# Optimization experiments

Hardware: AMD Instinct MI355X
Metric: run time of the kernel (lower is better)

The kernel has to match this reference:

```python
import jax, jax.numpy as jnp
import numpy as np

B=64; HW=14; E=2048; L=30; V=10000; EMB=512; AML=768; ADL=500
D=512+ADL   # decoder_dim + article_downlen = 1012
A=512+ADL   # attention_dim + article_downlen = 1012

def setup_inputs() -> dict:
    key = jax.random.key(0)
    ks = jax.random.split(key, 20)
    s = 0.02
    lin = lambda k, i, o: (jax.random.normal(k, (i, o), jnp.float32) * s)
    inp = {}
    inp['encoder_out'] = jax.random.normal(ks[0], (B, HW, HW, E), jnp.float32)
    inp['encoded_captions'] = jax.random.randint(ks[1], (B, L), 0, V)
    cl = jax.random.randint(ks[2], (B, 1), 2, L + 1)
    inp['caption_lengths'] = cl.at[0, 0].set(L)  # ensure max decode length == L-1
    inp['encoded_articles'] = jax.random.normal(ks[3], (B, 1, AML), jnp.float32)
    inp['article_lengths'] = jax.random.randint(ks[4], (B, 1), 1, AML)
    inp['blank_context'] = 0
    inp['E_emb'] = jax.random.uniform(ks[5], (V, EMB), jnp.float32, -0.1, 0.1)
    inp['W_par'] = lin(ks[6], AML, ADL); inp['b_par'] = jnp.zeros(ADL, jnp.float32)
    inp['W_enc'] = lin(ks[7], E, A);     inp['b_enc'] = jnp.zeros(A, jnp.float32)
    inp['W_dec'] = lin(ks[8], D, A);     inp['b_dec'] = jnp.zeros(A, jnp.float32)
    inp['W_full'] = lin(ks[9], A, 1);    inp['b_full'] = jnp.zeros(1, jnp.float32)
    inp['W_h'] = lin(ks[10], E + ADL, D); inp['b_h'] = jnp.zeros(D, jnp.float32)
    inp['W_c'] = lin(ks[11], E + ADL, D); inp['b_c'] = jnp.zeros(D, jnp.float32)
    inp['W_fb'] = lin(ks[12], D, E);      inp['b_fb'] = jnp.zeros(E, jnp.float32)
    inp['W_ih'] = lin(ks[13], EMB + E, 4 * D); inp['b_ih'] = jnp.zeros(4 * D, jnp.float32)
    inp['W_hh'] = lin(ks[14], D, 4 * D);       inp['b_hh'] = jnp.zeros(4 * D, jnp.float32)
    inp['W_fc'] = jax.random.uniform(ks[15], (D, V), jnp.float32, -0.1, 0.1)
    inp['b_fc'] = jnp.zeros(V, jnp.float32)
    return inp

def reference(encoder_out, encoded_captions, caption_lengths, encoded_articles,
              article_lengths, blank_context, E_emb, W_par, b_par, W_enc, b_enc,
              W_dec, b_dec, W_full, b_full, W_h, b_h, W_c, b_c, W_fb, b_fb,
              W_ih, b_ih, W_hh, b_hh, W_fc, b_fc):
    Bv = encoder_out.shape[0]
    enc = encoder_out.reshape(Bv, -1, encoder_out.shape[-1])  # (B, P, E)
    lens = caption_lengths[:, 0]
    sort_ind = jnp.argsort(-lens)
    lens = lens[sort_ind]
    enc = enc[sort_ind]
    caps = encoded_captions[sort_ind]
    arts = encoded_articles[sort_ind]
    emb = E_emb[caps]                                   # (B, L, EMB)
    context = (arts @ W_par + b_par)[:, 0, :]           # ParagraphEncoder -> (B, ADL)
    dec_in = jnp.concatenate([enc.mean(axis=1), context], axis=1)
    h0 = dec_in @ W_h + b_h
    c0 = dec_in @ W_c + b_c
    dlens = lens - 1
    att1 = enc @ W_enc + b_enc                          # loop-invariant, (B, P, A)
    T = emb.shape[1] - 1

    def step(carry, t):
        h, c = carry
        active = (dlens > t)[:, None]                   # prefix mask (sorted desc)
        att2 = h @ W_dec + b_dec
        scores = (jax.nn.relu(att1 + att2[:, None, :]) @ W_full)[..., 0] + b_full[0]
        alpha = jax.nn.softmax(scores, axis=1)          # (B, P)
        awe = jnp.einsum('bp,bpe->be', alpha, enc)
        awe = jax.nn.sigmoid(h @ W_fb + b_fb) * awe     # gated attention encoding
        x = jnp.concatenate([emb[:, t, :], awe], axis=1)
        gates = x @ W_ih + b_ih + h @ W_hh + b_hh       # torch LSTMCell, gate order i,f,g,o
        i, f, g, o = jnp.split(gates, 4, axis=1)
        c_new = jax.nn.sigmoid(f) * c + jax.nn.sigmoid(i) * jnp.tanh(g)
        h_new = jax.nn.sigmoid(o) * jnp.tanh(c_new)
        preds = jnp.where(active, h_new @ W_fc + b_fc, 0.0)
        alpha_m = jnp.where(active, alpha, 0.0)
        h = jnp.where(active, h_new, h)
        c = jnp.where(active, c_new, c)
        return (h, c), (preds, alpha_m)

    _, (preds, alphas) = jax.lax.scan(step, (h0, c0), jnp.arange(T))
    predictions = jnp.transpose(preds, (1, 0, 2))       # (B, T, V)
    alphas = jnp.transpose(alphas, (1, 0, 2))           # (B, T, P)
    return (predictions, caps, dlens, alphas, sort_ind)
```

## Files before the change

### kernel.cpp

```cpp
#include <hip/hip_runtime.h>
#include <math.h>

#define B_   64
#define P_   196
#define E_   2048
#define L_   30
#define T_   29
#define V_   10000
#define EMB_ 512
#define AML_ 768
#define ADL_ 500
#define D_   1012
#define A_   1012
#define G4_  4048
#define XK_  2560

typedef unsigned short u16;
typedef __attribute__((ext_vector_type(8))) short bf16x8;
typedef __attribute__((ext_vector_type(4))) float f32x4;

__device__ __forceinline__ float sigf(float x) { return 1.f / (1.f + __expf(-x)); }
__device__ __forceinline__ float tanhf_fast(float x) { return 1.f - 2.f / (__expf(2.f * x) + 1.f); }
__device__ __forceinline__ u16 f2bf(float f) {
    unsigned u = __float_as_uint(f);
    return (u16)((u + 0x7FFFu + ((u >> 16) & 1u)) >> 16);
}
__device__ __forceinline__ float bf2f(u16 v) { return __uint_as_float(((unsigned)v) << 16); }

__global__ void k_setup(const int* __restrict__ clen, const int* __restrict__ caps,
                        float* __restrict__ out_caps, float* __restrict__ out_dlens,
                        float* __restrict__ out_sind,
                        int* __restrict__ sort_ind, int* __restrict__ dlens_i,
                        int* __restrict__ nact, int* __restrict__ caps_s)
{
    __shared__ int lens[B_];
    int t = threadIdx.x;
    if (t < B_) lens[t] = clen[t];
    __syncthreads();
    if (t < B_) {
        int my = lens[t];
        int rank = 0;
        for (int j = 0; j < B_; ++j) {
            int lj = lens[j];
            if (lj > my || (lj == my && j < t)) rank++;
        }
        sort_ind[rank] = t;
    }
    __syncthreads();
    if (t < B_) {
        int orig = sort_ind[t];
        int dl = lens[orig] - 1;
        dlens_i[t] = dl;
        out_dlens[t] = (float)dl;
        out_sind[t] = (float)orig;
        for (int j = 0; j < L_; ++j) {
            int cv = caps[orig * L_ + j];
            caps_s[t * L_ + j] = cv;
            out_caps[t * L_ + j] = (float)cv;
        }
    }
    __syncthreads();
    if (t < T_) {
        int cnt = 0;
        for (int j = 0; j < B_; ++j) cnt += (dlens_i[j] > t) ? 1 : 0;
        nact[t] = cnt;
    }
}

__global__ void k_zero(float4* __restrict__ p, long n4)
{
    long i = (long)blockIdx.x * 256 + threadIdx.x;
    if (i < n4) p[i] = make_float4(0.f, 0.f, 0.f, 0.f);
}

__global__ void k_cvt_enc(const float* __restrict__ enc, const int* __restrict__ sort_ind,
                          u16* __restrict__ A_bf)
{
    int row = blockIdx.y;
    int b = row / 196, p = row - b * 196;
    int e4 = (blockIdx.x * 256 + threadIdx.x) * 4;
    const float* src = enc + ((long)sort_ind[b] * 196 + p) * E_ + e4;
    float4 v = *(const float4*)src;
    unsigned lo = (unsigned)f2bf(v.x) | ((unsigned)f2bf(v.y) << 16);
    unsigned hi = (unsigned)f2bf(v.z) | ((unsigned)f2bf(v.w) << 16);
    uint2 pk; pk.x = lo; pk.y = hi;
    *(uint2*)(A_bf + (long)row * E_ + e4) = pk;
}

__global__ void k_transpose(const float* __restrict__ src, u16* __restrict__ dst,
                            int K, int N, int Kp, int Np)
{
    __shared__ float tile[32][33];
    int n0 = blockIdx.x * 32, k0 = blockIdx.y * 32;
    int tx = threadIdx.x, ty = threadIdx.y;
    for (int r = ty; r < 32; r += 8) {
        int k = k0 + r, n = n0 + tx;
        tile[r][tx] = (k < K && n < N) ? src[(long)k * N + n] : 0.f;
    }
    __syncthreads();
    for (int r = ty; r < 32; r += 8) {
        int n = n0 + r, k = k0 + tx;
        if (n < Np && k < Kp) dst[(long)n * Kp + k] = f2bf(tile[tx][r]);
    }
}

__global__ void k_encmean(const float* __restrict__ enc, const int* __restrict__ sort_ind,
                          u16* __restrict__ dec_in)
{
    int b = blockIdx.y;
    int e = blockIdx.x * 256 + threadIdx.x;
    int orig = sort_ind[b];
    const float* src = enc + (long)orig * P_ * E_ + e;
    float s = 0.f;
    for (int p = 0; p < P_; ++p) s += src[(long)p * E_];
    dec_in[(long)b * XK_ + e] = f2bf(s * (1.f / 196.f));
}

__global__ void k_ctx(const float* __restrict__ arts, const float* __restrict__ W_par,
                      const float* __restrict__ b_par, const int* __restrict__ sort_ind,
                      u16* __restrict__ dec_in)
{
    int b = blockIdx.y;
    int k = blockIdx.x * 256 + threadIdx.x;
    if (k >= 512) return;
    float s = 0.f;
    if (k < ADL_) {
        int orig = sort_ind[b];
        const float* ar = arts + (long)orig * AML_;
        s = b_par[k];
        for (int m = 0; m < AML_; ++m) s = fmaf(ar[m], W_par[m * ADL_ + k], s);
    }
    dec_in[(long)b * XK_ + E_ + k] = f2bf(s);
}

__global__ void k_emb_all(const float* __restrict__ E_emb, const int* __restrict__ caps_s,
                          u16* __restrict__ emb_all)
{
    int t = blockIdx.x;
    int b = blockIdx.y;
    int tok = caps_s[b * L_ + t];
    for (int k = threadIdx.x; k < EMB_; k += 256)
        emb_all[((long)t * B_ + b) * EMB_ + k] = f2bf(E_emb[(long)tok * EMB_ + k]);
}

__global__ void __launch_bounds__(256) k_att1_mfma(
    const u16* __restrict__ A, const u16* __restrict__ W,
    const float* __restrict__ bias, u16* __restrict__ Yb)
{
    int w = threadIdx.x >> 6, lane = threadIdx.x & 63;
    int lr = lane & 15, lk = (lane >> 4) * 8;
    int n0 = blockIdx.x * 256 + w * 64;
    int r0 = blockIdx.y * 64;
    f32x4 acc[4][4];
#pragma unroll
    for (int i = 0; i < 4; ++i)
#pragma unroll
        for (int j = 0; j < 4; ++j) acc[i][j] = (f32x4){0.f, 0.f, 0.f, 0.f};
    const u16* ap = A + (long)(r0 + lr) * E_ + lk;
    const u16* wp = W + (long)(n0 + lr) * E_ + lk;
    for (int k = 0; k < E_; k += 32) {
        bf16x8 af[4], bf[4];
#pragma unroll
        for (int mt = 0; mt < 4; ++mt) af[mt] = *(const bf16x8*)(ap + (long)mt * 16 * E_ + k);
#pragma unroll
        for (int nt = 0; nt < 4; ++nt) bf[nt] = *(const bf16x8*)(wp + (long)nt * 16 * E_ + k);
#pragma unroll
        for (int mt = 0; mt < 4; ++mt)
#pragma unroll
            for (int nt = 0; nt < 4; ++nt)
                acc[mt][nt] = __builtin_amdgcn_mfma_f32_16x16x32_bf16(af[mt], bf[nt], acc[mt][nt], 0, 0, 0);
    }
#pragma unroll
    for (int mt = 0; mt < 4; ++mt) {
#pragma unroll
        for (int nt = 0; nt < 4; ++nt) {
            int n = n0 + nt * 16 + lr;
            float bv = (n < A_) ? bias[n] : 0.f;
#pragma unroll
            for (int j = 0; j < 4; ++j) {
                int row = r0 + mt * 16 + (lane >> 4) * 4 + j;
                u16 outv = (n < A_) ? f2bf(acc[mt][nt][j] + bv) : (u16)0;
                Yb[(long)row * 1024 + n] = outv;
            }
        }
    }
}

template <int ACT, int OUT, int PADZ>
__global__ void __launch_bounds__(256) k_skinny(
    const u16* __restrict__ A1, const u16* __restrict__ W1, int K1,
    const float* __restrict__ bias1, void* __restrict__ Yv,
    long ldY, long offY, int Nmax,
    const int* __restrict__ nact, int t)
{
    int Bact = (t >= 0) ? nact[t] : B_;
    if (Bact <= 0) return;
    int mmax = (Bact + 15) >> 4;
    int w = threadIdx.x >> 6, lane = threadIdx.x & 63;
    int lr = lane & 15, lk = (lane >> 4) * 8;
    int n0 = blockIdx.x * 64 + w * 16;
    f32x4 acc[4];
#pragma unroll
    for (int m = 0; m < 4; ++m) acc[m] = (f32x4){0.f, 0.f, 0.f, 0.f};

    int n = n0 + lr;
    int nc = n < Nmax ? n : Nmax - 1;
    const u16* a1p = A1 + (long)lr * K1 + lk;
    const u16* w1p = W1 + (long)nc * K1 + lk;
    for (int k = 0; k < K1; k += 32) {
        bf16x8 bw = *(const bf16x8*)(w1p + k);
#pragma unroll
        for (int m = 0; m < 4; ++m)
            if (m < mmax) {
                bf16x8 aw = *(const bf16x8*)(a1p + (long)m * 16 * K1 + k);
                acc[m] = __builtin_amdgcn_mfma_f32_16x16x32_bf16(aw, bw, acc[m], 0, 0, 0);
            }
    }
    float bv = (n < Nmax) ? bias1[n] : 0.f;
#pragma unroll
    for (int m = 0; m < 4; ++m) {
        if (m < mmax) {
#pragma unroll
            for (int j = 0; j < 4; ++j) {
                int b = m * 16 + (lane >> 4) * 4 + j;
                if (b < Bact) {
                    float v = acc[m][j] + bv;
                    if (ACT == 1) v = sigf(v);
                    if (n < Nmax) {
                        if (OUT == 1) ((u16*)Yv)[(long)b * ldY + offY + n] = f2bf(v);
                        else          ((float*)Yv)[(long)b * ldY + offY + n] = v;
                    } else if (PADZ) {
                        if (OUT == 1) ((u16*)Yv)[(long)b * ldY + offY + n] = 0;
                        else          ((float*)Yv)[(long)b * ldY + offY + n] = 0.f;
                    }
                }
            }
        }
    }
}

__global__ void __launch_bounds__(256) k_att2fb(
    const u16* __restrict__ h_bf, const u16* __restrict__ WT_dec,
    const u16* __restrict__ WT_fb, const float* __restrict__ b_dec,
    const float* __restrict__ b_fb, float* __restrict__ att2p,
    float* __restrict__ fbp, const int* __restrict__ nact, int t)
{
    int Bact = nact[t];
    if (Bact <= 0) return;
    int mmax = (Bact + 15) >> 4;
    int kh = blockIdx.x >= 48;
    int nb = blockIdx.x - (kh ? 48 : 0);
    int isfb = nb >= 16;
    const u16* W = isfb ? WT_fb : WT_dec;
    const float* bias = isfb ? b_fb : b_dec;
    int Nmax = isfb ? E_ : A_;
    int nb2 = isfb ? nb - 16 : nb;
    long ldY = isfb ? (long)E_ : 1024L;
    float* Y = (isfb ? fbp : att2p) + (long)kh * B_ * ldY;

    int w = threadIdx.x >> 6, lane = threadIdx.x & 63;
    int lr = lane & 15, lk = (lane >> 4) * 8;
    int n = nb2 * 64 + w * 16 + lr;
    int nc = n < Nmax ? n : Nmax - 1;
    int k0 = kh * 512;
    f32x4 acc[4];
#pragma unroll
    for (int m = 0; m < 4; ++m) acc[m] = (f32x4){0.f, 0.f, 0.f, 0.f};
    const u16* ap = h_bf + (long)lr * 1024 + k0 + lk;
    const u16* wp = W + (long)nc * 1024 + k0 + lk;
    for (int k = 0; k < 512; k += 32) {
        bf16x8 bw = *(const bf16x8*)(wp + k);
#pragma unroll
        for (int m = 0; m < 4; ++m)
            if (m < mmax) {
                bf16x8 aw = *(const bf16x8*)(ap + (long)m * 16 * 1024 + k);
                acc[m] = __builtin_amdgcn_mfma_f32_16x16x32_bf16(aw, bw, acc[m], 0, 0, 0);
            }
    }
    if (n >= Nmax) return;
    float bv = (kh == 0) ? bias[n] : 0.f;
#pragma unroll
    for (int m = 0; m < 4; ++m) {
        if (m < mmax) {
#pragma unroll
            for (int j = 0; j < 4; ++j) {
                int b = m * 16 + (lane >> 4) * 4 + j;
                if (b < Bact) Y[(long)b * ldY + n] = acc[m][j] + bv;
            }
        }
    }
}

__global__ void k_scores(const u16* __restrict__ att1, const float* __restrict__ att2p,
                         const float* __restrict__ W_full, const float* __restrict__ b_full,
                         float* __restrict__ scores, const int* __restrict__ nact, int t)
{
    int b = blockIdx.y;
    if (b >= nact[t]) return;
    int wv = threadIdx.x >> 6;
    int lane = threadIdx.x & 63;
    int p = blockIdx.x * 4 + wv;
    const u16* a1 = att1 + ((long)b * P_ + p) * 1024;
    const float* a20 = att2p + (long)b * 1024;
    const float* a21 = att2p + (long)B_ * 1024 + (long)b * 1024;
    float acc = 0.f;
    for (int j2 = lane; j2 < 506; j2 += 64) {
        unsigned pk = *(const unsigned*)(a1 + 2 * j2);
        float2 p0 = *(const float2*)(a20 + 2 * j2);
        float2 p1 = *(const float2*)(a21 + 2 * j2);
        float2 wv2 = *(const float2*)(W_full + 2 * j2);
        float v0 = bf2f((u16)(pk & 0xFFFF)) + p0.x + p1.x;
        float v1 = bf2f((u16)(pk >> 16)) + p0.y + p1.y;
        v0 = v0 > 0.f ? v0 : 0.f;
        v1 = v1 > 0.f ? v1 : 0.f;
        acc = fmaf(v0, wv2.x, acc);
        acc = fmaf(v1, wv2.y, acc);
    }
    for (int m = 32; m >= 1; m >>= 1) acc += __shfl_xor(acc, m);
    if (lane == 0) scores[b * P_ + p] = acc + b_full[0];
}

__global__ void __launch_bounds__(256) k_awe_x(
    const u16* __restrict__ A_bf, const float* __restrict__ scores,
    const float* __restrict__ fbp, u16* __restrict__ awe_buf,
    float* __restrict__ alphas_out, const int* __restrict__ nact, int t)
{
    int b = blockIdx.y;
    if (b >= nact[t]) return;
    int tid = threadIdx.x;
    int w = tid >> 6, lane = tid & 63;
    __shared__ float al[P_];
    __shared__ float red[4];
    float v = (tid < P_) ? scores[b * P_ + tid] : -1e30f;
    float m = v;
    for (int s = 32; s >= 1; s >>= 1) m = fmaxf(m, __shfl_xor(m, s));
    if (lane == 0) red[w] = m;
    __syncthreads();
    m = fmaxf(fmaxf(red[0], red[1]), fmaxf(red[2], red[3]));
    float e = (tid < P_) ? __expf(v - m) : 0.f;
    float s_ = e;
    for (int s = 32; s >= 1; s >>= 1) s_ += __shfl_xor(s_, s);
    __syncthreads();
    if (lane == 0) red[w] = s_;
    __syncthreads();
    s_ = red[0] + red[1] + red[2] + red[3];
    if (tid < P_) al[tid] = e / s_;
    __syncthreads();

    if (blockIdx.x < 8) {
        int e0 = blockIdx.x * 256 + tid;
        const u16* src = A_bf + (long)b * P_ * E_ + e0;
        float s0 = 0.f, s1 = 0.f, s2 = 0.f, s3 = 0.f;
        for (int p = 0; p < P_; p += 4) {
            s0 = fmaf(al[p],     bf2f(src[(long)p * E_]), s0);
            s1 = fmaf(al[p + 1], bf2f(src[(long)(p + 1) * E_]), s1);
            s2 = fmaf(al[p + 2], bf2f(src[(long)(p + 2) * E_]), s2);
            s3 = fmaf(al[p + 3], bf2f(src[(long)(p + 3) * E_]), s3);
        }
        float g = sigf(fbp[(long)b * E_ + e0] + fbp[(long)(B_ + b) * E_ + e0]);
        awe_buf[(long)b * E_ + e0] = f2bf((s0 + s1 + s2 + s3) * g);
    } else {
        if (tid < P_) alphas_out[((long)b * T_ + t) * P_ + tid] = al[tid];
    }
}

__global__ void __launch_bounds__(256) k_gates(
    const u16* __restrict__ emb_t, const u16* __restrict__ awe,
    const u16* __restrict__ h_old, const u16* __restrict__ WT_ih,
    const u16* __restrict__ WT_hh, float* __restrict__ gpart,
    const int* __restrict__ nact, int t)
{
    int Bact = nact[t];
    if (Bact <= 0) return;
    int mmax = (Bact + 15) >> 4;
    int q = threadIdx.x >> 6;
    int lane = threadIdx.x & 63;
    int lr = lane & 15, lk = (lane >> 4) * 8;
    int kh = blockIdx.y;
    int n = blockIdx.x * 16 + lr;
    int nc = n < D_ ? n : D_ - 1;
    f32x4 acc[4];
#pragma unroll
    for (int m = 0; m < 4; ++m) acc[m] = (f32x4){0.f, 0.f, 0.f, 0.f};
    const u16* wih = WT_ih + ((long)q * D_ + nc) * XK_;
    const u16* whh = WT_hh + ((long)q * D_ + nc) * 1024;

    if (kh == 0) {
        const u16* ap = emb_t + (long)lr * EMB_ + lk;
        for (int k = 0; k < EMB_; k += 32) {
            bf16x8 bw = *(const bf16x8*)(wih + k);
#pragma unroll
            for (int m = 0; m < 4; ++m)
                if (m < mmax) {
                    bf16x8 aw = *(const bf16x8*)(ap + (long)m * 16 * EMB_ + k);
                    acc[m] = __builtin_amdgcn_mfma_f32_16x16x32_bf16(aw, bw, acc[m], 0, 0, 0);
                }
        }
        const u16* ap2 = awe + (long)lr * E_ + lk;
        const u16* w2 = wih + EMB_;
        for (int k = 0; k < 1280; k += 32) {
            bf16x8 bw = *(const bf16x8*)(w2 + k);
#pragma unroll
            for (int m = 0; m < 4; ++m)
                if (m < mmax) {
                    bf16x8 aw = *(const bf16x8*)(ap2 + (long)m * 16 * E_ + k);
                    acc[m] = __builtin_amdgcn_mfma_f32_16x16x32_bf16(aw, bw, acc[m], 0, 0, 0);
                }
        }
    } else {
        const u16* ap2 = awe + (long)lr * E_ + 1280 + lk;
        const u16* w2 = wih + 1792;
        for (int k = 0; k < 768; k += 32) {
            bf16x8 bw = *(const bf16x8*)(w2 + k);
#pragma unroll
            for (int m = 0; m < 4; ++m)
                if (m < mmax) {
                    bf16x8 aw = *(const bf16x8*)(ap2 + (long)m * 16 * E_ + k);
                    acc[m] = __builtin_amdgcn_mfma_f32_16x16x32_bf16(aw, bw, acc[m], 0, 0, 0);
                }
        }
        const u16* ap3 = h_old + (long)lr * 1024 + lk;
        for (int k = 0; k < 1024; k += 32) {
            bf16x8 bw = *(const bf16x8*)(whh + k);
#pragma unroll
            for (int m = 0; m < 4; ++m)
                if (m < mmax) {
                    bf16x8 aw = *(const bf16x8*)(ap3 + (long)m * 16 * 1024 + k);
                    acc[m] = __builtin_amdgcn_mfma_f32_16x16x32_bf16(aw, bw, acc[m], 0, 0, 0);
                }
        }
    }
#pragma unroll
    for (int m = 0; m < 4; ++m) {
        if (m < mmax) {
#pragma unroll
            for (int j = 0; j < 4; ++j) {
                int bb = m * 16 + (lane >> 4) * 4 + j;
                if (bb < Bact)
                    gpart[((long)kh * B_ + bb) * 4096 + q * 1024 + n] = acc[m][j];
            }
        }
    }
}

__global__ void k_lstm_red(const float* __restrict__ gpart, const float* __restrict__ b_ih,
                           const float* __restrict__ b_hh, float* __restrict__ cbuf,
                           u16* __restrict__ h_new, const int* __restrict__ nact, int t)
{
    int b = blockIdx.y;
    if (b >= nact[t]) return;
    int n = blockIdx.x * 256 + threadIdx.x;
    if (n >= D_) return;
    const float* g0 = gpart + (long)b * 4096;
    const float* g1 = gpart + (long)(B_ + b) * 4096;
    float gi = g0[n]        + g1[n]        + b_ih[n]          + b_hh[n];
    float gf = g0[1024 + n] + g1[1024 + n] + b_ih[D_ + n]     + b_hh[D_ + n];
    float gg = g0[2048 + n] + g1[2048 + n] + b_ih[2 * D_ + n] + b_hh[2 * D_ + n];
    float go = g0[3072 + n] + g1[3072 + n] + b_ih[3 * D_ + n] + b_hh[3 * D_ + n];
    float c = cbuf[(long)b * 1024 + n];
    float cn = sigf(gf) * c + sigf(gi) * tanhf_fast(gg);
    float hn = sigf(go) * tanhf_fast(cn);
    cbuf[(long)b * 1024 + n] = cn;
    h_new[(long)b * 1024 + n] = f2bf(hn);
}

__global__ void __launch_bounds__(256) k_fc_all(
    const u16* __restrict__ h_all, const u16* __restrict__ W,
    const float* __restrict__ bias, float* __restrict__ out_preds,
    const int* __restrict__ nact)
{
    int tslot = blockIdx.y;
    int Bact = nact[tslot];
    if (Bact <= 0) return;
    int mmax = (Bact + 15) >> 4;
    int w = threadIdx.x >> 6, lane = threadIdx.x & 63;
    int lr = lane & 15, lk = (lane >> 4) * 8;
    int n0 = blockIdx.x * 256 + w * 64;
    f32x4 acc[4][4];
#pragma unroll
    for (int i = 0; i < 4; ++i)
#pragma unroll
        for (int j = 0; j < 4; ++j) acc[i][j] = (f32x4){0.f, 0.f, 0.f, 0.f};
    const u16* ap = h_all + ((long)(tslot + 1) * B_ + lr) * 1024 + lk;
    int ncl[4];
#pragma unroll
    for (int nt = 0; nt < 4; ++nt) {
        int n = n0 + nt * 16 + lr;
        ncl[nt] = n < V_ ? n : V_ - 1;
    }
    for (int k = 0; k < 1024; k += 32) {
        bf16x8 af[4], bf[4];
#pragma unroll
        for (int mt = 0; mt < 4; ++mt)
            if (mt < mmax) af[mt] = *(const bf16x8*)(ap + (long)mt * 16 * 1024 + k);
#pragma unroll
        for (int nt = 0; nt < 4; ++nt) bf[nt] = *(const bf16x8*)(W + (long)ncl[nt] * 1024 + lk + k);
#pragma unroll
        for (int mt = 0; mt < 4; ++mt)
            if (mt < mmax)
#pragma unroll
                for (int nt = 0; nt < 4; ++nt)
                    acc[mt][nt] = __builtin_amdgcn_mfma_f32_16x16x32_bf16(af[mt], bf[nt], acc[mt][nt], 0, 0, 0);
    }
#pragma unroll
    for (int nt = 0; nt < 4; ++nt) {
        int n = n0 + nt * 16 + lr;
        if (n >= V_) continue;
        float bv = bias[n];
#pragma unroll
        for (int mt = 0; mt < 4; ++mt) {
            if (mt < mmax) {
#pragma unroll
                for (int j = 0; j < 4; ++j) {
                    int b = mt * 16 + (lane >> 4) * 4 + j;
                    if (b < Bact)
                        out_preds[(long)b * T_ * V_ + (long)tslot * V_ + n] = acc[mt][nt][j] + bv;
                }
            }
        }
    }
}

extern "C" void kernel_launch(void* const* d_in, const int* in_sizes, int n_in,
                              void* d_out, int out_size, void* d_ws, size_t ws_size,
                              hipStream_t stream)
{
    const float* enc    = (const float*)d_in[0];
    const int*   caps   = (const int*)d_in[1];
    const int*   clen   = (const int*)d_in[2];
    const float* arts   = (const float*)d_in[3];
    const float* E_emb  = (const float*)d_in[6];
    const float* W_par  = (const float*)d_in[7];
    const float* b_par  = (const float*)d_in[8];
    const float* W_enc  = (const float*)d_in[9];
    const float* b_enc  = (const float*)d_in[10];
    const float* W_dec  = (const float*)d_in[11];
    const float* b_dec  = (const float*)d_in[12];
    const float* W_full = (const float*)d_in[13];
    const float* b_full = (const float*)d_in[14];
    const float* W_h    = (const float*)d_in[15];
    const float* b_h    = (const float*)d_in[16];
    const float* W_c    = (const float*)d_in[17];
    const float* b_c    = (const float*)d_in[18];
    const float* W_fb   = (const float*)d_in[19];
    const float* b_fb   = (const float*)d_in[20];
    const float* W_ih   = (const float*)d_in[21];
    const float* b_ih   = (const float*)d_in[22];
    const float* W_hh   = (const float*)d_in[23];
    const float* b_hh   = (const float*)d_in[24];
    const float* W_fc   = (const float*)d_in[25];
    const float* b_fc   = (const float*)d_in[26];

    float* out = (float*)d_out;
    float* out_preds  = out;
    float* out_caps   = out + (long)B_ * T_ * V_;
    float* out_dlens  = out_caps + B_ * L_;
    float* out_alphas = out_dlens + B_;
    float* out_sind   = out_alphas + (long)B_ * T_ * P_;

    float* ws = (float*)d_ws;
    long o = 0;
    auto alloc = [&](long n) { long r = o; o += (n + 63) & ~63L; return r; };
    long o_ints   = alloc(2176);
    long o_decin  = alloc((long)B_ * XK_ / 2);
    long o_hall   = alloc((long)(T_ + 1) * B_ * 1024 / 2);
    long o_emball = alloc((long)T_ * B_ * EMB_ / 2);
    long o_awe    = alloc((long)B_ * E_ / 2);
    long o_c      = alloc((long)B_ * 1024);
    long o_att2p  = alloc((long)2 * B_ * 1024);
    long o_fbp    = alloc((long)2 * B_ * E_);
    long o_gpart  = alloc((long)2 * B_ * 4096);
    long o_scores = alloc((long)B_ * P_);
    long o_Abf    = alloc((long)12544 * E_ / 2);
    long o_att1   = alloc((long)12544 * 1024 / 2);
    long o_wtenc  = alloc((long)1024 * 2048 / 2);
    long o_wtdec  = alloc((long)1024 * 1024 / 2);
    long o_wtfb   = alloc((long)2048 * 1024 / 2);
    long o_wtih   = alloc((long)4096 * 2560 / 2);
    long o_wthh   = alloc((long)4096 * 1024 / 2);
    long o_wtfc   = alloc((long)10048 * 1024 / 2);

    int* sort_ind = (int*)(ws + o_ints);
    int* dlens_i  = sort_ind + 64;
    int* nact     = dlens_i + 64;
    int* caps_s   = nact + 32;
    u16*   dec_in  = (u16*)(ws + o_decin);
    u16*   h_all   = (u16*)(ws + o_hall);
    u16*   emb_all = (u16*)(ws + o_emball);
    u16*   awe_buf = (u16*)(ws + o_awe);
    float* cbuf   = ws + o_c;
    float* att2p  = ws + o_att2p;
    float* fbp    = ws + o_fbp;
    float* gpart  = ws + o_gpart;
    float* scores = ws + o_scores;
    u16*   A_bf   = (u16*)(ws + o_Abf);
    u16*   att1   = (u16*)(ws + o_att1);
    u16*   WT_enc = (u16*)(ws + o_wtenc);
    u16*   WT_dec = (u16*)(ws + o_wtdec);
    u16*   WT_fb  = (u16*)(ws + o_wtfb);
    u16*   WT_ih  = (u16*)(ws + o_wtih);
    u16*   WT_hh  = (u16*)(ws + o_wthh);
    u16*   WT_fc  = (u16*)(ws + o_wtfc);
    u16*   WT_h   = att1;
    u16*   WT_c   = att1 + (long)1024 * XK_;

    long n4 = ((long)B_ * T_ * V_ + B_ * L_ + B_ + (long)B_ * T_ * P_ + B_) / 4;
    k_zero<<<dim3((unsigned)((n4 + 255) / 256)), 256, 0, stream>>>((float4*)d_out, n4);
    k_setup<<<1, 64, 0, stream>>>(clen, caps, out_caps, out_dlens, out_sind,
                                  sort_ind, dlens_i, nact, caps_s);

    k_encmean<<<dim3(8, 64), 256, 0, stream>>>(enc, sort_ind, dec_in);
    k_ctx<<<dim3(2, 64), 256, 0, stream>>>(arts, W_par, b_par, sort_ind, dec_in);
    k_emb_all<<<dim3(T_, 64), 256, 0, stream>>>(E_emb, caps_s, emb_all);

    dim3 tb(32, 8);
    k_transpose<<<dim3(1024/32, 2560/32), tb, 0, stream>>>(W_h, WT_h, 2548, 1012, 2560, 1024);
    k_transpose<<<dim3(1024/32, 2560/32), tb, 0, stream>>>(W_c, WT_c, 2548, 1012, 2560, 1024);
    k_skinny<0,1,1><<<dim3(16), 256, 0, stream>>>(dec_in, WT_h, XK_, b_h, h_all, 1024L, 0L, D_,
                                                  nact, -1);
    k_skinny<0,0,1><<<dim3(16), 256, 0, stream>>>(dec_in, WT_c, XK_, b_c, cbuf, 1024L, 0L, D_,
                                                  nact, -1);

    k_transpose<<<dim3(1024/32, 2048/32), tb, 0, stream>>>(W_enc, WT_enc, 2048, 1012, 2048, 1024);
    k_transpose<<<dim3(1024/32, 1024/32), tb, 0, stream>>>(W_dec, WT_dec, 1012, 1012, 1024, 1024);
    k_transpose<<<dim3(2048/32, 1024/32), tb, 0, stream>>>(W_fb, WT_fb, 1012, 2048, 1024, 2048);
    k_transpose<<<dim3(4096/32, 2560/32), tb, 0, stream>>>(W_ih, WT_ih, 2560, 4048, 2560, 4096);
    k_transpose<<<dim3(4096/32, 1024/32), tb, 0, stream>>>(W_hh, WT_hh, 1012, 4048, 1024, 4096);
    k_transpose<<<dim3(10048/32, 1024/32), tb, 0, stream>>>(W_fc, WT_fc, 1012, 10000, 1024, 10048);

    k_cvt_enc<<<dim3(2, 12544), 256, 0, stream>>>(enc, sort_ind, A_bf);
    k_att1_mfma<<<dim3(4, 196), 256, 0, stream>>>(A_bf, WT_enc, b_enc, att1);

    for (int t = 0; t < T_; ++t) {
        const u16* h_old = h_all + (long)t * B_ * 1024;
        u16* h_new = h_all + (long)(t + 1) * B_ * 1024;
        const u16* emb_t = emb_all + (long)t * B_ * EMB_;
        k_att2fb<<<dim3(96), 256, 0, stream>>>(h_old, WT_dec, WT_fb, b_dec, b_fb,
                                               att2p, fbp, nact, t);
        k_scores<<<dim3(49, 64), 256, 0, stream>>>(att1, att2p, W_full, b_full, scores, nact, t);
        k_awe_x<<<dim3(9, 64), 256, 0, stream>>>(A_bf, scores, fbp, awe_buf,
                                                 out_alphas, nact, t);
        k_gates<<<dim3(64, 2), 256, 0, stream>>>(emb_t, awe_buf, h_old, WT_ih, WT_hh,
                                                 gpart, nact, t);
        k_lstm_red<<<dim3(4, 64), 256, 0, stream>>>(gpart, b_ih, b_hh, cbuf, h_new, nact, t);
    }
    k_fc_all<<<dim3(40, T_), 256, 0, stream>>>(h_all, WT_fc, b_fc, out_preds, nact);
}
```

Measured before the change: 3.111 ms.

## Precompute embedding gate contributions for all steps; stage att1 A tiles in LDS

The embedding part of the LSTM input projection (emb @ W_ih[:512]) does not depend on the recurrence, so it is now computed for all timesteps in one batched MFMA kernel before the loop. The per-step gate kernel only handles the attention-weighted encoding and hidden-state terms, with its K split rebalanced between the two block halves, and the LSTM reduction adds the precomputed term. The att1 GEMM now double-buffers A tiles through shared memory so the four waves share them instead of each loading them from global memory. The cost is an extra T*B*4096 float workspace and extra synchronisation in the att1 loop.

Result: faster. 2.847 ms (-8.5%).

```diff
diff --git a/kernel.cpp b/kernel.cpp
--- a/kernel.cpp
+++ b/kernel.cpp
@@ -147,28 +147,42 @@
     const u16* __restrict__ A, const u16* __restrict__ W,
     const float* __restrict__ bias, u16* __restrict__ Yb)
 {
+    __shared__ u16 As[2][64][40];
     int w = threadIdx.x >> 6, lane = threadIdx.x & 63;
     int lr = lane & 15, lk = (lane >> 4) * 8;
     int n0 = blockIdx.x * 256 + w * 64;
     int r0 = blockIdx.y * 64;
+    int arow = threadIdx.x >> 2;
+    int akseg = (threadIdx.x & 3) * 8;
+    const u16* ag = A + (long)(r0 + arow) * E_ + akseg;
+
     f32x4 acc[4][4];
 #pragma unroll
     for (int i = 0; i < 4; ++i)
 #pragma unroll
         for (int j = 0; j < 4; ++j) acc[i][j] = (f32x4){0.f, 0.f, 0.f, 0.f};
-    const u16* ap = A + (long)(r0 + lr) * E_ + lk;
     const u16* wp = W + (long)(n0 + lr) * E_ + lk;
+
+    *(uint2*)&As[0][arow][akseg] = *(const uint2*)(ag);
+    __syncthreads();
+
     for (int k = 0; k < E_; k += 32) {
-        bf16x8 af[4], bf[4];
-#pragma unroll
-        for (int mt = 0; mt < 4; ++mt) af[mt] = *(const bf16x8*)(ap + (long)mt * 16 * E_ + k);
+        int buf = (k >> 5) & 1;
+        bool more = (k + 32) < E_;
+        uint2 pre;
+        if (more) pre = *(const uint2*)(ag + k + 32);
+        bf16x8 bf[4], af[4];
 #pragma unroll
         for (int nt = 0; nt < 4; ++nt) bf[nt] = *(const bf16x8*)(wp + (long)nt * 16 * E_ + k);
+#pragma unroll
+        for (int mt = 0; mt < 4; ++mt) af[mt] = *(const bf16x8*)&As[buf][mt * 16 + lr][lk];
 #pragma unroll
         for (int mt = 0; mt < 4; ++mt)
 #pragma unroll
             for (int nt = 0; nt < 4; ++nt)
                 acc[mt][nt] = __builtin_amdgcn_mfma_f32_16x16x32_bf16(af[mt], bf[nt], acc[mt][nt], 0, 0, 0);
+        if (more) *(uint2*)&As[buf ^ 1][arow][akseg] = pre;
+        __syncthreads();
     }
 #pragma unroll
     for (int mt = 0; mt < 4; ++mt) {
@@ -234,6 +248,53 @@
                         else          ((float*)Yv)[(long)b * ldY + offY + n] = 0.f;
                     }
                 }
+            }
+        }
+    }
+}
+
+__global__ void __launch_bounds__(256) k_gemb(
+    const u16* __restrict__ emb_all, const u16* __restrict__ WT_ih,
+    float* __restrict__ gemb_all)
+{
+    int t = blockIdx.y;
+    int w = threadIdx.x >> 6, lane = threadIdx.x & 63;
+    int lr = lane & 15, lk = (lane >> 4) * 8;
+    int n0 = blockIdx.x * 256 + w * 64;
+    f32x4 acc[4][4];
+#pragma unroll
+    for (int i = 0; i < 4; ++i)
+#pragma unroll
+        for (int j = 0; j < 4; ++j) acc[i][j] = (f32x4){0.f, 0.f, 0.f, 0.f};
+    const u16* ap = emb_all + ((long)t * B_ + lr) * EMB_ + lk;
+    long wrow[4];
+#pragma unroll
+    for (int nt = 0; nt < 4; ++nt) {
+        int j = n0 + nt * 16 + lr;
+        int q = j >> 10, d = j & 1023;
+        wrow[nt] = (long)q * D_ + (d < D_ ? d : D_ - 1);
+    }
+    for (int k = 0; k < EMB_; k += 32) {
+        bf16x8 af[4], bf[4];
+#pragma unroll
+        for (int mt = 0; mt < 4; ++mt) af[mt] = *(const bf16x8*)(ap + (long)mt * 16 * EMB_ + k);
+#pragma unroll
+        for (int nt = 0; nt < 4; ++nt) bf[nt] = *(const bf16x8*)(WT_ih + wrow[nt] * XK_ + lk + k);
+#pragma unroll
+        for (int mt = 0; mt < 4; ++mt)
+#pragma unroll
+            for (int nt = 0; nt < 4; ++nt)
+                acc[mt][nt] = __builtin_amdgcn_mfma_f32_16x16x32_bf16(af[mt], bf[nt], acc[mt][nt], 0, 0, 0);
+    }
+#pragma unroll
+    for (int nt = 0; nt < 4; ++nt) {
+        int j = n0 + nt * 16 + lr;
+#pragma unroll
+        for (int mt = 0; mt < 4; ++mt) {
+#pragma unroll
+            for (int jj = 0; jj < 4; ++jj) {
+                int b = mt * 16 + (lane >> 4) * 4 + jj;
+                gemb_all[((long)t * B_ + b) * 4096 + j] = acc[mt][nt][jj];
             }
         }
     }
@@ -357,7 +418,8 @@
             s2 = fmaf(al[p + 2], bf2f(src[(long)(p + 2) * E_]), s2);
             s3 = fmaf(al[p + 3], bf2f(src[(long)(p + 3) * E_]), s3);
         }
-        float g = sigf(fbp[(long)b * E_ + e0] + fbp[(long)(B_ + b) * E_ + e0]);
+        long fb_off = (long)b * E_ + e0;
+        float g = sigf(fbp[fb_off] + fbp[131072 + fb_off]);
         awe_buf[(long)b * E_ + e0] = f2bf((s0 + s1 + s2 + s3) * g);
     } else {
         if (tid < P_) alphas_out[((long)b * T_ + t) * P_ + tid] = al[tid];
@@ -365,10 +427,9 @@
 }
 
 __global__ void __launch_bounds__(256) k_gates(
-    const u16* __restrict__ emb_t, const u16* __restrict__ awe,
-    const u16* __restrict__ h_old, const u16* __restrict__ WT_ih,
-    const u16* __restrict__ WT_hh, float* __restrict__ gpart,
-    const int* __restrict__ nact, int t)
+    const u16* __restrict__ awe, const u16* __restrict__ h_old,
+    const u16* __restrict__ WT_ih, const u16* __restrict__ WT_hh,
+    float* __restrict__ gpart, const int* __restrict__ nact, int t)
 {
     int Bact = nact[t];
     if (Bact <= 0) return;
@@ -386,19 +447,21 @@
     const u16* whh = WT_hh + ((long)q * D_ + nc) * 1024;
 
     if (kh == 0) {
-        const u16* ap = emb_t + (long)lr * EMB_ + lk;
-        for (int k = 0; k < EMB_; k += 32) {
-            bf16x8 bw = *(const bf16x8*)(wih + k);
+        const u16* ap = awe + (long)lr * E_ + lk;
+        const u16* w2 = wih + 512;
+        for (int k = 0; k < 1536; k += 32) {
+            bf16x8 bw = *(const bf16x8*)(w2 + k);
 #pragma unroll
             for (int m = 0; m < 4; ++m)
                 if (m < mmax) {
-                    bf16x8 aw = *(const bf16x8*)(ap + (long)m * 16 * EMB_ + k);
+                    bf16x8 aw = *(const bf16x8*)(ap + (long)m * 16 * E_ + k);
                     acc[m] = __builtin_amdgcn_mfma_f32_16x16x32_bf16(aw, bw, acc[m], 0, 0, 0);
                 }
         }
-        const u16* ap2 = awe + (long)lr * E_ + lk;
-        const u16* w2 = wih + EMB_;
-        for (int k = 0; k < 1280; k += 32) {
+    } else {
+        const u16* ap2 = awe + (long)lr * E_ + 1536 + lk;
+        const u16* w2 = wih + 2048;
+        for (int k = 0; k < 512; k += 32) {
             bf16x8 bw = *(const bf16x8*)(w2 + k);
 #pragma unroll
             for (int m = 0; m < 4; ++m)
@@ -407,18 +470,6 @@
                     acc[m] = __builtin_amdgcn_mfma_f32_16x16x32_bf16(aw, bw, acc[m], 0, 0, 0);
                 }
         }
-    } else {
-        const u16* ap2 = awe + (long)lr * E_ + 1280 + lk;
-        const u16* w2 = wih + 1792;
-        for (int k = 0; k < 768; k += 32) {
-            bf16x8 bw = *(const bf16x8*)(w2 + k);
-#pragma unroll
-            for (int m = 0; m < 4; ++m)
-                if (m < mmax) {
-                    bf16x8 aw = *(const bf16x8*)(ap2 + (long)m * 16 * E_ + k);
-                    acc[m] = __builtin_amdgcn_mfma_f32_16x16x32_bf16(aw, bw, acc[m], 0, 0, 0);
-                }
-        }
         const u16* ap3 = h_old + (long)lr * 1024 + lk;
         for (int k = 0; k < 1024; k += 32) {
             bf16x8 bw = *(const bf16x8*)(whh + k);
@@ -443,9 +494,10 @@
     }
 }
 
-__global__ void k_lstm_red(const float* __restrict__ gpart, const float* __restrict__ b_ih,
-                           const float* __restrict__ b_hh, float* __restrict__ cbuf,
-                           u16* __restrict__ h_new, const int* __restrict__ nact, int t)
+__global__ void k_lstm_red(const float* __restrict__ gpart, const float* __restrict__ gemb_t,
+                           const float* __restrict__ b_ih, const float* __restrict__ b_hh,
+                           float* __restrict__ cbuf, u16* __restrict__ h_new,
+                           const int* __restrict__ nact, int t)
 {
     int b = blockIdx.y;
     if (b >= nact[t]) return;
@@ -453,10 +505,11 @@
     if (n >= D_) return;
     const float* g0 = gpart + (long)b * 4096;
     const float* g1 = gpart + (long)(B_ + b) * 4096;
-    float gi = g0[n]        + g1[n]        + b_ih[n]          + b_hh[n];
-    float gf = g0[1024 + n] + g1[1024 + n] + b_ih[D_ + n]     + b_hh[D_ + n];
-    float gg = g0[2048 + n] + g1[2048 + n] + b_ih[2 * D_ + n] + b_hh[2 * D_ + n];
-    float go = g0[3072 + n] + g1[3072 + n] + b_ih[3 * D_ + n] + b_hh[3 * D_ + n];
+    const float* ge = gemb_t + (long)b * 4096;
+    float gi = g0[n]        + g1[n]        + ge[n]        + b_ih[n]          + b_hh[n];
+    float gf = g0[1024 + n] + g1[1024 + n] + ge[1024 + n] + b_ih[D_ + n]     + b_hh[D_ + n];
+    float gg = g0[2048 + n] + g1[2048 + n] + ge[2048 + n] + b_ih[2 * D_ + n] + b_hh[2 * D_ + n];
+    float go = g0[3072 + n] + g1[3072 + n] + ge[3072 + n] + b_ih[3 * D_ + n] + b_hh[3 * D_ + n];
     float c = cbuf[(long)b * 1024 + n];
     float cn = sigf(gf) * c + sigf(gi) * tanhf_fast(gg);
     float hn = sigf(go) * tanhf_fast(cn);
@@ -570,6 +623,7 @@
     long o_att2p  = alloc((long)2 * B_ * 1024);
     long o_fbp    = alloc((long)2 * B_ * E_);
     long o_gpart  = alloc((long)2 * B_ * 4096);
+    long o_gemb   = alloc((long)T_ * B_ * 4096);
     long o_scores = alloc((long)B_ * P_);
     long o_Abf    = alloc((long)12544 * E_ / 2);
     long o_att1   = alloc((long)12544 * 1024 / 2);
@@ -592,6 +646,7 @@
     float* att2p  = ws + o_att2p;
     float* fbp    = ws + o_fbp;
     float* gpart  = ws + o_gpart;
+    float* gemb_all = ws + o_gemb;
     float* scores = ws + o_scores;
     u16*   A_bf   = (u16*)(ws + o_Abf);
     u16*   att1   = (u16*)(ws + o_att1);
@@ -630,19 +685,20 @@
 
     k_cvt_enc<<<dim3(2, 12544), 256, 0, stream>>>(enc, sort_ind, A_bf);
     k_att1_mfma<<<dim3(4, 196), 256, 0, stream>>>(A_bf, WT_enc, b_enc, att1);
+    k_gemb<<<dim3(16, T_), 256, 0, stream>>>(emb_all, WT_ih, gemb_all);
 
     for (int t = 0; t < T_; ++t) {
         const u16* h_old = h_all + (long)t * B_ * 1024;
         u16* h_new = h_all + (long)(t + 1) * B_ * 1024;
-        const u16* emb_t = emb_all + (long)t * B_ * EMB_;
+        const float* gemb_t = gemb_all + (long)t * B_ * 4096;
         k_att2fb<<<dim3(96), 256, 0, stream>>>(h_old, WT_dec, WT_fb, b_dec, b_fb,
                                                att2p, fbp, nact, t);
         k_scores<<<dim3(49, 64), 256, 0, stream>>>(att1, att2p, W_full, b_full, scores, nact, t);
         k_awe_x<<<dim3(9, 64), 256, 0, stream>>>(A_bf, scores, fbp, awe_buf,
                                                  out_alphas, nact, t);
-        k_gates<<<dim3(64, 2), 256, 0, stream>>>(emb_t, awe_buf, h_old, WT_ih, WT_hh,
-                                                 gpart, nact, t);
-        k_lstm_red<<<dim3(4, 64), 256, 0, stream>>>(gpart, b_ih, b_hh, cbuf, h_new, nact, t);
+        k_gates<<<dim3(64, 2), 256, 0, stream>>>(awe_buf, h_old, WT_ih, WT_hh, gpart, nact, t);
+        k_lstm_red<<<dim3(4, 64), 256, 0, stream>>>(gpart, gemb_t, b_ih, b_hh, cbuf, h_new,
+                                                    nact, t);
     }
     k_fc_all<<<dim3(40, T_), 256, 0, stream>>>(h_all, WT_fc, b_fc, out_preds, nact);
 }
```
